# Kernel tuning notes

Measured on AMD Instinct MI355X. Metric: run time of the kernel, lower is better.

Reference implementation:

```python
import jax, jax.numpy as jnp
from jax import lax
import numpy as np

T = 8192
D = 10000
L_CONV = T - 18          # after two valid convs with kernel 10
L_POOL = L_CONV // 2     # after MaxPool1d(2)
FLAT = 128 * L_POOL      # flattened feature size fed to the on-the-fly Linear
TWO_PI = 6.283185307179586

# feat indices used by feat_emb[0..17], in emb order
FEAT_IDX = np.array([558, 582, 554, 552, 93, 555, 580, 571, 574, 578,
                     566, 287, 556, 550, 14, 551, 64, 581], dtype=np.int32)


def setup_inputs() -> dict:
    key = jax.random.key(0)
    ks = jax.random.split(key, 12)
    inp = {
        "signals": jax.random.normal(ks[0], (T, 4), jnp.float32),
        "feat": jax.random.normal(ks[1], (600,), jnp.float32),
        "conv1_w": jax.random.normal(ks[2], (64, 4, 10), jnp.float32) * 0.15,
        "conv1_b": jax.random.normal(ks[3], (64,), jnp.float32) * 0.05,
        "conv2_w": jax.random.normal(ks[4], (128, 64, 10), jnp.float32) * 0.04,
        "conv2_b": jax.random.normal(ks[5], (128,), jnp.float32) * 0.05,
        "lin_w": jax.random.normal(ks[6], (128, FLAT), jnp.float32) * (1.0 / np.sqrt(FLAT)),
        "lin_b": jax.random.normal(ks[7], (128,), jnp.float32) * 0.05,
        "hdc_w": jax.random.normal(ks[8], (D, 128), jnp.float32),  # Sinusoid weight ~ N(0,1)
        "hdc_b": jax.random.uniform(ks[9], (D,), jnp.float32, 0.0, TWO_PI),
        "feat_w": jax.random.normal(ks[10], (18, D), jnp.float32),  # 18 Sinusoid(1, D) weights
        "feat_b": jax.random.uniform(ks[11], (18, D), jnp.float32, 0.0, TWO_PI),
        "feat_idx": jnp.asarray(FEAT_IDX),
    }
    return inp


def _sinusoid(proj, bias):
    # torchhd Sinusoid: cos(xW^T + b) * sin(xW^T)
    return jnp.cos(proj + bias) * jnp.sin(proj)


def reference(signals, feat, conv1_w, conv1_b, conv2_w, conv2_b,
              lin_w, lin_b, hdc_w, hdc_b, feat_w, feat_b, feat_idx):
    # CNN front-end (dropout is identity in eval mode)
    x = signals.T[None]  # [1, 4, T]
    dn = ('NCH', 'OIH', 'NCH')
    x = lax.conv_general_dilated(x, conv1_w, (1,), 'VALID', dimension_numbers=dn)
    x = jax.nn.relu(x + conv1_b[None, :, None])
    x = lax.conv_general_dilated(x, conv2_w, (1,), 'VALID', dimension_numbers=dn)
    x = jax.nn.relu(x + conv2_b[None, :, None])  # [1, 128, L_CONV]
    L = x.shape[2] // 2
    x = x[:, :, :L * 2].reshape(1, 128, L, 2).max(axis=-1)  # MaxPool1d(2)
    x = x.reshape(1, -1)                                     # [1, FLAT]
    x = jax.nn.relu(x @ lin_w.T + lin_b)                     # [1, 128]

    # sample hypervector
    proj = x @ hdc_w.T                                       # [1, D]
    sample_hv = _sinusoid(proj, hdc_b)

    # 18 per-feature sinusoid embeddings, vectorized: proj_i = feat[idx_i] * w_i
    fvals = feat[feat_idx]                                   # [18]
    fproj = fvals[:, None] * feat_w                          # [18, D]
    h = _sinusoid(fproj, feat_b)                             # [18, D]

    feat_hv = ((h[14] + h[11]) * h[16]
               * (h[4] + h[8] + h[6] + h[1] + h[5] + h[12] + h[17])
               * h[13] * (h[15] + h[2]) * h[3]
               * h[0] * h[10] * h[7] * h[9])                 # [D]

    combined = sample_hv + feat_hv[None]                     # [1, D]
    quantized = jnp.where(combined > 0, 1.0, -1.0).astype(combined.dtype)
    return quantized.reshape(-1)                             # [D]
```

## Files before the change

### kernel.cpp

```cpp
#include <hip/hip_runtime.h>
#include <math.h>

#define T_IN    8192
#define T1      8183
#define LP      4087
#define NFLAT   523136
#define NFLAT4  130784
#define NDIM    10000
#define RSTRIDE 8208
#define F_OFF   (64*RSTRIDE)
#define P_OFF   (F_OFF + NFLAT)
#define NCHUNK  32
#define CHUNK4  4087

typedef __attribute__((ext_vector_type(4))) float f4;

__global__ __launch_bounds__(256) void k1_conv1(
    const float* __restrict__ sig, const float* __restrict__ w1,
    const float* __restrict__ b1, float* __restrict__ r1)
{
  __shared__ float4 srow[266];
  const int tid = threadIdx.x;
  const int t0b = blockIdx.x * 256;
  for (int idx = tid; idx < 266; idx += 256) {
    int t = t0b + idx;
    float4 v = make_float4(0.f, 0.f, 0.f, 0.f);
    if (t < T_IN) v = ((const float4*)sig)[t];
    srow[idx] = v;
  }
  __syncthreads();
  const int t = t0b + tid;
  float s[40];
#pragma unroll
  for (int k = 0; k < 10; ++k) {
    float4 v = srow[tid + k];
    s[4*k+0] = v.x; s[4*k+1] = v.y; s[4*k+2] = v.z; s[4*k+3] = v.w;
  }
  const int c0 = blockIdx.y * 8;
  for (int c = c0; c < c0 + 8; ++c) {
    const float* __restrict__ w = w1 + c * 40;
    float a0 = 0.f, a1 = 0.f, a2 = 0.f, a3 = 0.f;
#pragma unroll
    for (int k = 0; k < 10; ++k) {
      a0 = fmaf(s[4*k+0], w[k     ], a0);
      a1 = fmaf(s[4*k+1], w[10 + k], a1);
      a2 = fmaf(s[4*k+2], w[20 + k], a2);
      a3 = fmaf(s[4*k+3], w[30 + k], a3);
    }
    float v = fmaxf((a0 + a1) + (a2 + a3) + b1[c], 0.f);
    if (t < T1) r1[c * RSTRIDE + t] = v;
  }
}

__global__ __launch_bounds__(256) void k2_conv2pool(
    const float* __restrict__ r1, const float* __restrict__ w2,
    const float* __restrict__ b2, float* __restrict__ flat)
{
  const int tid  = threadIdx.x;
  const int lane = tid & 63;
  const int wave = tid >> 6;
  const int t0b  = blockIdx.x * 256;
  const int o0   = __builtin_amdgcn_readfirstlane(blockIdx.y * 8 + wave * 2);
  const int t0   = t0b + lane * 4;

  float acc[2][4];
#pragma unroll
  for (int a = 0; a < 2; ++a)
#pragma unroll
    for (int b = 0; b < 4; ++b) acc[a][b] = 0.f;

  for (int c = 0; c < 64; ++c) {
    const f4* __restrict__ p = (const f4*)(r1 + c * RSTRIDE + t0b) + lane;
    f4 v0 = p[0];
    f4 v1 = p[1];
    f4 v2 = p[2];
    f4 v3 = p[3];
    float f[16];
    f[0]=v0.x; f[1]=v0.y; f[2]=v0.z; f[3]=v0.w;
    f[4]=v1.x; f[5]=v1.y; f[6]=v1.z; f[7]=v1.w;
    f[8]=v2.x; f[9]=v2.y; f[10]=v2.z; f[11]=v2.w;
    f[12]=v3.x; f[13]=v3.y; f[14]=v3.z; f[15]=v3.w;
#pragma unroll
    for (int oo = 0; oo < 2; ++oo) {
      const float* __restrict__ w = w2 + ((o0 + oo) * 64 + c) * 10;
#pragma unroll
      for (int k = 0; k < 10; ++k) {
        float wv = w[k];
#pragma unroll
        for (int tt = 0; tt < 4; ++tt)
          acc[oo][tt] = fmaf(wv, f[k + tt], acc[oo][tt]);
      }
    }
  }

#pragma unroll
  for (int oo = 0; oo < 2; ++oo) {
    const int o = o0 + oo;
    const float bias = b2[o];
#pragma unroll
    for (int lt = 0; lt < 2; ++lt) {
      float a = acc[oo][2*lt]     + bias;
      float b = acc[oo][2*lt + 1] + bias;
      float m = fmaxf(fmaxf(a, b), 0.f);
      int l = t0 / 2 + lt;
      if (l < LP) flat[o * LP + l] = m;
    }
  }
}

__global__ __launch_bounds__(256) void k3_linear(
    const float* __restrict__ lw, const float* __restrict__ flat,
    float* __restrict__ partials)
{
  const int tid = threadIdx.x;
  const int ch  = blockIdx.x;
  const int j0  = blockIdx.y * 4;
  const f4* __restrict__ fl = (const f4*)flat + (size_t)ch * CHUNK4;

  float r[4];
#pragma unroll
  for (int ph = 0; ph < 2; ++ph) {
    const int j = j0 + 2 * ph;
    const f4* __restrict__ p0 = (const f4*)lw + (size_t)(j + 0) * NFLAT4 + (size_t)ch * CHUNK4;
    const f4* __restrict__ p1 = (const f4*)lw + (size_t)(j + 1) * NFLAT4 + (size_t)ch * CHUNK4;
    f4 a0 = (f4)0.f, a1 = (f4)0.f;
    for (int i = tid; i < CHUNK4; i += 256) {
      f4 x  = fl[i];
      f4 w0 = p0[i];
      f4 w1 = p1[i];
      a0.x = fmaf(x.x, w0.x, a0.x); a0.y = fmaf(x.y, w0.y, a0.y);
      a0.z = fmaf(x.z, w0.z, a0.z); a0.w = fmaf(x.w, w0.w, a0.w);
      a1.x = fmaf(x.x, w1.x, a1.x); a1.y = fmaf(x.y, w1.y, a1.y);
      a1.z = fmaf(x.z, w1.z, a1.z); a1.w = fmaf(x.w, w1.w, a1.w);
    }
    r[2*ph + 0] = (a0.x + a0.y) + (a0.z + a0.w);
    r[2*ph + 1] = (a1.x + a1.y) + (a1.z + a1.w);
  }

  __shared__ float red[4][257];
#pragma unroll
  for (int j = 0; j < 4; ++j) red[j][tid] = r[j];
  for (int off = 128; off > 0; off >>= 1) {
    __syncthreads();
    if (tid < off) {
#pragma unroll
      for (int j = 0; j < 4; ++j) red[j][tid] += red[j][tid + off];
    }
  }
  if (tid == 0) {
#pragma unroll
    for (int j = 0; j < 4; ++j) partials[(j0 + j) * NCHUNK + ch] = red[j][0];
  }
}

__global__ __launch_bounds__(64) void k4_hdc(
    const float* __restrict__ partials, const float* __restrict__ lin_b,
    const float* __restrict__ hdc_w, const float* __restrict__ hdc_b,
    const float* __restrict__ feat, const int* __restrict__ feat_idx,
    const float* __restrict__ feat_w, const float* __restrict__ feat_b,
    float* __restrict__ out)
{
  __shared__ __align__(16) float y[128];
  __shared__ float fv[18];
  const int tid = threadIdx.x;
#pragma unroll
  for (int half = 0; half < 2; ++half) {
    const int row = tid + half * 64;
    float s = lin_b[row];
    const float* p = partials + row * NCHUNK;
#pragma unroll
    for (int c = 0; c < NCHUNK; ++c) s += p[c];
    y[row] = fmaxf(s, 0.f);
  }
  if (tid < 18) fv[tid] = feat[feat_idx[tid]];
  __syncthreads();

  const int d = blockIdx.x * 64 + tid;
  if (d >= NDIM) return;

  const float4* __restrict__ hw = (const float4*)(hdc_w + d * 128);
  const float4* __restrict__ yy = (const float4*)y;
  float4 ac = make_float4(0, 0, 0, 0);
#pragma unroll
  for (int q = 0; q < 32; ++q) {
    float4 w = hw[q];
    float4 v = yy[q];
    ac.x = fmaf(w.x, v.x, ac.x); ac.y = fmaf(w.y, v.y, ac.y);
    ac.z = fmaf(w.z, v.z, ac.z); ac.w = fmaf(w.w, v.w, ac.w);
  }
  const float proj = (ac.x + ac.y) + (ac.z + ac.w);
  const float sample_hv = cosf(proj + hdc_b[d]) * sinf(proj);

  float h[18];
#pragma unroll
  for (int i = 0; i < 18; ++i) {
    float fp = fv[i] * feat_w[i * NDIM + d];
    h[i] = cosf(fp + feat_b[i * NDIM + d]) * sinf(fp);
  }
  const float feat_hv =
      (h[14] + h[11]) * h[16]
    * (h[4] + h[8] + h[6] + h[1] + h[5] + h[12] + h[17])
    * h[13] * (h[15] + h[2]) * h[3]
    * h[0] * h[10] * h[7] * h[9];

  const float comb = sample_hv + feat_hv;
  out[d] = comb > 0.f ? 1.f : -1.f;
}

extern "C" void kernel_launch(void* const* d_in, const int* in_sizes, int n_in,
                              void* d_out, int out_size, void* d_ws, size_t ws_size,
                              hipStream_t stream)
{
  const float* sig  = (const float*)d_in[0];
  const float* feat = (const float*)d_in[1];
  const float* w1   = (const float*)d_in[2];
  const float* b1   = (const float*)d_in[3];
  const float* w2   = (const float*)d_in[4];
  const float* b2   = (const float*)d_in[5];
  const float* lw   = (const float*)d_in[6];
  const float* lb   = (const float*)d_in[7];
  const float* hw   = (const float*)d_in[8];
  const float* hb   = (const float*)d_in[9];
  const float* fw   = (const float*)d_in[10];
  const float* fb   = (const float*)d_in[11];
  const int*   fidx = (const int*)d_in[12];
  float* out = (float*)d_out;
  float* ws  = (float*)d_ws;

  float* r1       = ws;
  float* flat     = ws + F_OFF;
  float* partials = ws + P_OFF;

  k1_conv1    <<<dim3(32, 8),  256, 0, stream>>>(sig, w1, b1, r1);
  k2_conv2pool<<<dim3(32, 16), 256, 0, stream>>>(r1, w2, b2, flat);
  k3_linear   <<<dim3(32, 32), 256, 0, stream>>>(lw, flat, partials);
  k4_hdc      <<<dim3(157, 1), 64,  0, stream>>>(partials, lb, hw, hb,
                                                 feat, fidx, fw, fb, out);
}
```

Baseline: 95.44 us.

## Fuse four kernels into one cooperative persistent kernel with grid syncs

Replaces the four separate launches with a single cooperative kernel that runs conv1, conv2, pooling, linear and the HDC stage in phases separated by grid.sync. Conv2 is split across two channel halves writing partial sums, followed by a separate pooling/bias/ReLU pass, which raises the number of parallel blocks. The aim is to remove launch gaps between kernels and to occupy more CUs during conv2. In exchange it adds grid-wide barrier costs and an extra round trip through global memory for the partial sums, and it falls back to the old kernels if the cooperative launch fails.

```diff
diff --git a/kernel.cpp b/kernel.cpp
--- a/kernel.cpp
+++ b/kernel.cpp
@@ -1,19 +1,233 @@
 #include <hip/hip_runtime.h>
+#include <hip/hip_cooperative_groups.h>
 #include <math.h>
+
+namespace cg = cooperative_groups;
 
 #define T_IN    8192
 #define T1      8183
+#define T2      8174
 #define LP      4087
 #define NFLAT   523136
 #define NFLAT4  130784
 #define NDIM    10000
 #define RSTRIDE 8208
-#define F_OFF   (64*RSTRIDE)
+#define PROW    8192
+#define PA_OFF  (64*RSTRIDE)
+#define F_OFF   (PA_OFF + 2*128*PROW)
 #define P_OFF   (F_OFF + NFLAT)
 #define NCHUNK  32
 #define CHUNK4  4087
+#define NVB     1024
 
 typedef __attribute__((ext_vector_type(4))) float f4;
+typedef __attribute__((ext_vector_type(2))) float f2;
+
+__global__ __launch_bounds__(256, 4) void mega(
+    const float* __restrict__ sig,  const float* __restrict__ feat,
+    const float* __restrict__ w1,   const float* __restrict__ b1,
+    const float* __restrict__ w2,   const float* __restrict__ b2,
+    const float* __restrict__ lw,   const float* __restrict__ lb,
+    const float* __restrict__ hwm,  const float* __restrict__ hb,
+    const float* __restrict__ fw,   const float* __restrict__ fb,
+    const int* __restrict__ fidx,
+    float* __restrict__ ws,         float* __restrict__ out)
+{
+  cg::grid_group grid = cg::this_grid();
+  float* r1       = ws;
+  float* pacc     = ws + PA_OFF;
+  float* flat     = ws + F_OFF;
+  float* partials = ws + P_OFF;
+
+  const int tid  = threadIdx.x;
+  const int b    = blockIdx.x;
+  const int nb   = gridDim.x;
+  const int lane = tid & 63;
+  const int wave = tid >> 6;
+
+  __shared__ float4 srow[266];
+  __shared__ float  red[4][257];
+  __shared__ __align__(16) float ybuf[128];
+  __shared__ float  fv[18];
+
+  for (int vb = b; vb < NVB; vb += nb) {
+    __syncthreads();
+    const int t0b = (vb & 31) * 256;
+    const int c0  = (vb >> 5) * 2;
+    for (int idx = tid; idx < 266; idx += 256) {
+      int t = t0b + idx;
+      float4 v = make_float4(0.f, 0.f, 0.f, 0.f);
+      if (t < T_IN) v = ((const float4*)sig)[t];
+      srow[idx] = v;
+    }
+    __syncthreads();
+    const int t = t0b + tid;
+    float s[40];
+#pragma unroll
+    for (int k = 0; k < 10; ++k) {
+      float4 v = srow[tid + k];
+      s[4*k+0] = v.x; s[4*k+1] = v.y; s[4*k+2] = v.z; s[4*k+3] = v.w;
+    }
+#pragma unroll
+    for (int cc = 0; cc < 2; ++cc) {
+      const int c = c0 + cc;
+      const float* __restrict__ w = w1 + c * 40;
+      float a0 = 0.f, a1 = 0.f, a2 = 0.f, a3 = 0.f;
+#pragma unroll
+      for (int k = 0; k < 10; ++k) {
+        a0 = fmaf(s[4*k+0], w[k     ], a0);
+        a1 = fmaf(s[4*k+1], w[10 + k], a1);
+        a2 = fmaf(s[4*k+2], w[20 + k], a2);
+        a3 = fmaf(s[4*k+3], w[30 + k], a3);
+      }
+      float v = fmaxf((a0 + a1) + (a2 + a3) + b1[c], 0.f);
+      if (t < T1) r1[c * RSTRIDE + t] = v;
+    }
+  }
+  grid.sync();
+
+  for (int vb = b; vb < NVB; vb += nb) {
+    const int t0b = (vb & 31) * 256;
+    const int o0  = __builtin_amdgcn_readfirstlane(((vb >> 5) & 15) * 8 + wave * 2);
+    const int cb  = (vb >> 9) * 32;
+
+    float acc[2][4];
+#pragma unroll
+    for (int a = 0; a < 2; ++a)
+#pragma unroll
+      for (int q = 0; q < 4; ++q) acc[a][q] = 0.f;
+
+    for (int ci = 0; ci < 32; ++ci) {
+      const int c = cb + ci;
+      const f4* __restrict__ p = (const f4*)(r1 + c * RSTRIDE + t0b) + lane;
+      f4 v0 = p[0];
+      f4 v1 = p[1];
+      f4 v2 = p[2];
+      f4 v3 = p[3];
+      float f[16];
+      f[0]=v0.x; f[1]=v0.y; f[2]=v0.z; f[3]=v0.w;
+      f[4]=v1.x; f[5]=v1.y; f[6]=v1.z; f[7]=v1.w;
+      f[8]=v2.x; f[9]=v2.y; f[10]=v2.z; f[11]=v2.w;
+      f[12]=v3.x; f[13]=v3.y; f[14]=v3.z; f[15]=v3.w;
+#pragma unroll
+      for (int oo = 0; oo < 2; ++oo) {
+        const float* __restrict__ w = w2 + ((o0 + oo) * 64 + c) * 10;
+#pragma unroll
+        for (int k = 0; k < 10; ++k) {
+          float wv = w[k];
+#pragma unroll
+          for (int q = 0; q < 4; ++q)
+            acc[oo][q] = fmaf(wv, f[k + q], acc[oo][q]);
+        }
+      }
+    }
+#pragma unroll
+    for (int oo = 0; oo < 2; ++oo) {
+      f4 v; v.x = acc[oo][0]; v.y = acc[oo][1]; v.z = acc[oo][2]; v.w = acc[oo][3];
+      *(f4*)(pacc + (size_t)((vb >> 9) * 128 + o0 + oo) * PROW + t0b + lane * 4) = v;
+    }
+  }
+  grid.sync();
+
+  for (unsigned idx = (unsigned)b * 256u + tid; idx < NFLAT; idx += (unsigned)nb * 256u) {
+    const unsigned o = idx / (unsigned)LP;
+    const unsigned l = idx - o * (unsigned)LP;
+    const unsigned t = 2u * l;
+    f2 x0 = *(const f2*)(pacc + (size_t)o * PROW + t);
+    f2 x1 = *(const f2*)(pacc + (size_t)(128 + o) * PROW + t);
+    const float bias = b2[o];
+    float aa = (x0.x + x1.x) + bias;
+    float bb = (x0.y + x1.y) + bias;
+    flat[idx] = fmaxf(fmaxf(aa, bb), 0.f);
+  }
+  grid.sync();
+
+  for (int vb = b; vb < NVB; vb += nb) {
+    __syncthreads();
+    const int ch = vb & 31;
+    const int j0 = (vb >> 5) * 4;
+    const f4* __restrict__ fl = (const f4*)flat + (size_t)ch * CHUNK4;
+
+    float r[4];
+#pragma unroll
+    for (int ph = 0; ph < 2; ++ph) {
+      const int j = j0 + 2 * ph;
+      const f4* __restrict__ p0 = (const f4*)lw + (size_t)(j + 0) * NFLAT4 + (size_t)ch * CHUNK4;
+      const f4* __restrict__ p1 = (const f4*)lw + (size_t)(j + 1) * NFLAT4 + (size_t)ch * CHUNK4;
+      f4 a0 = (f4)0.f, a1 = (f4)0.f;
+      for (int i = tid; i < CHUNK4; i += 256) {
+        f4 x  = fl[i];
+        f4 w0 = p0[i];
+        f4 w1 = p1[i];
+        a0.x = fmaf(x.x, w0.x, a0.x); a0.y = fmaf(x.y, w0.y, a0.y);
+        a0.z = fmaf(x.z, w0.z, a0.z); a0.w = fmaf(x.w, w0.w, a0.w);
+        a1.x = fmaf(x.x, w1.x, a1.x); a1.y = fmaf(x.y, w1.y, a1.y);
+        a1.z = fmaf(x.z, w1.z, a1.z); a1.w = fmaf(x.w, w1.w, a1.w);
+      }
+      r[2*ph + 0] = (a0.x + a0.y) + (a0.z + a0.w);
+      r[2*ph + 1] = (a1.x + a1.y) + (a1.z + a1.w);
+    }
+
+#pragma unroll
+    for (int j = 0; j < 4; ++j) red[j][tid] = r[j];
+    for (int off = 128; off > 0; off >>= 1) {
+      __syncthreads();
+      if (tid < off) {
+#pragma unroll
+        for (int j = 0; j < 4; ++j) red[j][tid] += red[j][tid + off];
+      }
+    }
+    if (tid == 0) {
+#pragma unroll
+      for (int j = 0; j < 4; ++j) partials[(j0 + j) * NCHUNK + ch] = red[j][0];
+    }
+  }
+  grid.sync();
+
+  for (int vb = b; vb < 40; vb += nb) {
+    __syncthreads();
+    if (tid < 128) {
+      float s = lb[tid];
+      const float* p = partials + tid * NCHUNK;
+#pragma unroll
+      for (int c = 0; c < NCHUNK; ++c) s += p[c];
+      ybuf[tid] = fmaxf(s, 0.f);
+    }
+    if (tid < 18) fv[tid] = feat[fidx[tid]];
+    __syncthreads();
+
+    const int d = vb * 256 + tid;
+    if (d < NDIM) {
+      const float4* __restrict__ hwp = (const float4*)(hwm + d * 128);
+      const float4* __restrict__ yy  = (const float4*)ybuf;
+      float4 ac = make_float4(0, 0, 0, 0);
+#pragma unroll
+      for (int q = 0; q < 32; ++q) {
+        float4 w = hwp[q];
+        float4 v = yy[q];
+        ac.x = fmaf(w.x, v.x, ac.x); ac.y = fmaf(w.y, v.y, ac.y);
+        ac.z = fmaf(w.z, v.z, ac.z); ac.w = fmaf(w.w, v.w, ac.w);
+      }
+      const float proj = (ac.x + ac.y) + (ac.z + ac.w);
+      const float sample_hv = cosf(proj + hb[d]) * sinf(proj);
+
+      float h[18];
+#pragma unroll
+      for (int i = 0; i < 18; ++i) {
+        float fp = fv[i] * fw[i * NDIM + d];
+        h[i] = cosf(fp + fb[i * NDIM + d]) * sinf(fp);
+      }
+      const float feat_hv =
+          (h[14] + h[11]) * h[16]
+        * (h[4] + h[8] + h[6] + h[1] + h[5] + h[12] + h[17])
+        * h[13] * (h[15] + h[2]) * h[3]
+        * h[0] * h[10] * h[7] * h[9];
+
+      const float comb = sample_hv + feat_hv;
+      out[d] = comb > 0.f ? 1.f : -1.f;
+    }
+  }
+}
 
 __global__ __launch_bounds__(256) void k1_conv1(
     const float* __restrict__ sig, const float* __restrict__ w1,
@@ -67,7 +281,7 @@
 #pragma unroll
   for (int a = 0; a < 2; ++a)
 #pragma unroll
-    for (int b = 0; b < 4; ++b) acc[a][b] = 0.f;
+    for (int q = 0; q < 4; ++q) acc[a][q] = 0.f;
 
   for (int c = 0; c < 64; ++c) {
     const f4* __restrict__ p = (const f4*)(r1 + c * RSTRIDE + t0b) + lane;
@@ -100,8 +314,8 @@
 #pragma unroll
     for (int lt = 0; lt < 2; ++lt) {
       float a = acc[oo][2*lt]     + bias;
-      float b = acc[oo][2*lt + 1] + bias;
-      float m = fmaxf(fmaxf(a, b), 0.f);
+      float bq = acc[oo][2*lt + 1] + bias;
+      float m = fmaxf(fmaxf(a, bq), 0.f);
       int l = t0 / 2 + lt;
       if (l < LP) flat[o * LP + l] = m;
     }
@@ -227,13 +441,30 @@
   float* out = (float*)d_out;
   float* ws  = (float*)d_ws;
 
-  float* r1       = ws;
-  float* flat     = ws + F_OFF;
-  float* partials = ws + P_OFF;
-
-  k1_conv1    <<<dim3(32, 8),  256, 0, stream>>>(sig, w1, b1, r1);
-  k2_conv2pool<<<dim3(32, 16), 256, 0, stream>>>(r1, w2, b2, flat);
-  k3_linear   <<<dim3(32, 32), 256, 0, stream>>>(lw, flat, partials);
-  k4_hdc      <<<dim3(157, 1), 64,  0, stream>>>(partials, lb, hw, hb,
-                                                 feat, fidx, fw, fb, out);
-}
+  int nblk = 0;
+  hipError_t oe = hipOccupancyMaxActiveBlocksPerMultiprocessor(
+      &nblk, (const void*)mega, 256, 0);
+  int gsz = NVB;
+  if (oe == hipSuccess && nblk > 0) {
+    long cap = (long)nblk * 256;
+    if (cap < gsz) gsz = (int)cap;
+  }
+
+  void* args[] = { (void*)&sig, (void*)&feat, (void*)&w1, (void*)&b1,
+                   (void*)&w2,  (void*)&b2,   (void*)&lw, (void*)&lb,
+                   (void*)&hw,  (void*)&hb,   (void*)&fw, (void*)&fb,
+                   (void*)&fidx, (void*)&ws,  (void*)&out };
+  hipError_t err = hipLaunchCooperativeKernel((const void*)mega, dim3(gsz),
+                                              dim3(256), args, 0, stream);
+  if (err != hipSuccess) {
+    (void)hipGetLastError();
+    float* r1       = ws;
+    float* flat     = ws + F_OFF;
+    float* partials = ws + P_OFF;
+    k1_conv1    <<<dim3(32, 8),  256, 0, stream>>>(sig, w1, b1, r1);
+    k2_conv2pool<<<dim3(32, 16), 256, 0, stream>>>(r1, w2, b2, flat);
+    k3_linear   <<<dim3(32, 32), 256, 0, stream>>>(lw, flat, partials);
+    k4_hdc      <<<dim3(157, 1), 64,  0, stream>>>(partials, lb, hw, hb,
+                                                   feat, fidx, fw, fb, out);
+  }
+}
```

Measured after the change: 349.9 us. 267% more time.

## Split conv2 input channels across two blocks with separate combine kernel

Applied to the files above, without the earlier changes.

Conv2 is split along the input-channel dimension into two halves, which doubles the block count (1024 instead of 512) so more of the GPU is occupied. Each half writes its partial sums to a workspace buffer. A new combine kernel adds the two halves, applies bias, ReLU and max-pool, and writes the flattened features. This costs an extra kernel launch and roughly 8 MB of extra global writes and reads.

```diff
diff --git a/kernel.cpp b/kernel.cpp
--- a/kernel.cpp
+++ b/kernel.cpp
@@ -8,12 +8,15 @@
 #define NFLAT4  130784
 #define NDIM    10000
 #define RSTRIDE 8208
-#define F_OFF   (64*RSTRIDE)
+#define PROW    8192
+#define PA_OFF  (64*RSTRIDE)
+#define F_OFF   (PA_OFF + 2*128*PROW)
 #define P_OFF   (F_OFF + NFLAT)
 #define NCHUNK  32
 #define CHUNK4  4087
 
 typedef __attribute__((ext_vector_type(4))) float f4;
+typedef __attribute__((ext_vector_type(2))) float f2;
 
 __global__ __launch_bounds__(256) void k1_conv1(
     const float* __restrict__ sig, const float* __restrict__ w1,
@@ -52,24 +55,27 @@
   }
 }
 
-__global__ __launch_bounds__(256) void k2_conv2pool(
+__global__ __launch_bounds__(256) void k2a_conv2part(
     const float* __restrict__ r1, const float* __restrict__ w2,
-    const float* __restrict__ b2, float* __restrict__ flat)
+    float* __restrict__ pacc)
 {
   const int tid  = threadIdx.x;
   const int lane = tid & 63;
   const int wave = tid >> 6;
   const int t0b  = blockIdx.x * 256;
   const int o0   = __builtin_amdgcn_readfirstlane(blockIdx.y * 8 + wave * 2);
-  const int t0   = t0b + lane * 4;
+  const int h    = blockIdx.z;
+  const int cb   = h * 32;
 
   float acc[2][4];
 #pragma unroll
   for (int a = 0; a < 2; ++a)
 #pragma unroll
-    for (int b = 0; b < 4; ++b) acc[a][b] = 0.f;
-
-  for (int c = 0; c < 64; ++c) {
+    for (int q = 0; q < 4; ++q) acc[a][q] = 0.f;
+
+#pragma unroll 2
+  for (int ci = 0; ci < 32; ++ci) {
+    const int c = cb + ci;
     const f4* __restrict__ p = (const f4*)(r1 + c * RSTRIDE + t0b) + lane;
     f4 v0 = p[0];
     f4 v1 = p[1];
@@ -95,15 +101,29 @@
 
 #pragma unroll
   for (int oo = 0; oo < 2; ++oo) {
-    const int o = o0 + oo;
-    const float bias = b2[o];
-#pragma unroll
-    for (int lt = 0; lt < 2; ++lt) {
-      float a = acc[oo][2*lt]     + bias;
-      float b = acc[oo][2*lt + 1] + bias;
-      float m = fmaxf(fmaxf(a, b), 0.f);
-      int l = t0 / 2 + lt;
-      if (l < LP) flat[o * LP + l] = m;
+    f4 v; v.x = acc[oo][0]; v.y = acc[oo][1]; v.z = acc[oo][2]; v.w = acc[oo][3];
+    *(f4*)(pacc + (size_t)(h * 128 + o0 + oo) * PROW + t0b + lane * 4) = v;
+  }
+}
+
+__global__ __launch_bounds__(256) void k2b_combine(
+    const float* __restrict__ pacc, const float* __restrict__ b2,
+    float* __restrict__ flat)
+{
+  const unsigned gtid = blockIdx.x * 256u + threadIdx.x;
+#pragma unroll
+  for (int e = 0; e < 2; ++e) {
+    const unsigned idx = gtid + e * 262144u;
+    if (idx < NFLAT) {
+      const unsigned o = idx / (unsigned)LP;
+      const unsigned l = idx - o * (unsigned)LP;
+      const unsigned t = 2u * l;
+      f2 x0 = *(const f2*)(pacc + (size_t)o * PROW + t);
+      f2 x1 = *(const f2*)(pacc + (size_t)(128 + o) * PROW + t);
+      const float bias = b2[o];
+      float aa = (x0.x + x1.x) + bias;
+      float bb = (x0.y + x1.y) + bias;
+      flat[idx] = fmaxf(fmaxf(aa, bb), 0.f);
     }
   }
 }
@@ -228,12 +248,14 @@
   float* ws  = (float*)d_ws;
 
   float* r1       = ws;
+  float* pacc     = ws + PA_OFF;
   float* flat     = ws + F_OFF;
   float* partials = ws + P_OFF;
 
-  k1_conv1    <<<dim3(32, 8),  256, 0, stream>>>(sig, w1, b1, r1);
-  k2_conv2pool<<<dim3(32, 16), 256, 0, stream>>>(r1, w2, b2, flat);
-  k3_linear   <<<dim3(32, 32), 256, 0, stream>>>(lw, flat, partials);
-  k4_hdc      <<<dim3(157, 1), 64,  0, stream>>>(partials, lb, hw, hb,
-                                                 feat, fidx, fw, fb, out);
-}
+  k1_conv1    <<<dim3(32, 8),     256, 0, stream>>>(sig, w1, b1, r1);
+  k2a_conv2part<<<dim3(32, 16, 2), 256, 0, stream>>>(r1, w2, pacc);
+  k2b_combine <<<dim3(1024),      256, 0, stream>>>(pacc, b2, flat);
+  k3_linear   <<<dim3(32, 32),    256, 0, stream>>>(lw, flat, partials);
+  k4_hdc      <<<dim3(157, 1),    64,  0, stream>>>(partials, lb, hw, hb,
+                                                    feat, fidx, fw, fb, out);
+}
```

Measured after the change: 88.26 us. 7.5% less time.
